# Performance work log

Measured on AMD Instinct MI355X. Metric: run time of the kernel, lower is better.

## Reference

```python
import jax, jax.numpy as jnp
import numpy as np

B, H, S, D = 8, 16, 1024, 64  # batch, heads, seq, projection_size = state_size // n_heads
SCALE = 1.0 / float(np.sqrt(D))


def setup_inputs() -> dict:
    key = jax.random.key(0)
    kq, kk, kv, kl = jax.random.split(key, 4)
    q = jax.random.normal(kq, (B, H, S, D), jnp.float32)
    k = jax.random.normal(kk, (B, H, S, D), jnp.float32)
    v = jax.random.normal(kv, (B, H, S, D), jnp.float32)
    # causal position mask: True = masked (filled with -inf), as in masked_fill
    position_mask = jnp.triu(jnp.ones((S, S), dtype=bool), k=1)
    # per-batch source lengths in [S//2, S]; mask positions >= length
    lengths = jax.random.randint(kl, (B,), S // 2, S + 1)
    src_length_mask = jnp.arange(S)[None, :] >= lengths[:, None]  # [B, S]
    return {"q": q, "k": k, "v": v,
            "position_mask": position_mask,
            "src_length_mask": src_length_mask}


def reference(q, q_unused=None, *, _=None, **__):
    raise RuntimeError  # placeholder (replaced below)


def reference(q, k, v, position_mask, src_length_mask):
    # scores = scale * Q K^T   (torch: bmm over [B*H, S, D]; here kept 4D, same math)
    logits = jnp.einsum('bhqd,bhkd->bhqk', q, k) * SCALE  # [B,H,Sq,Sk]
    neg_inf = jnp.array(-jnp.inf, dtype=logits.dtype)
    # apply_logit_masks: position mask broadcasts over [B,H],
    # src_length_mask viewed as [B,1,1,Sk]
    logits = jnp.where(position_mask[None, None, :, :], neg_inf, logits)
    logits = jnp.where(src_length_mask[:, None, None, :], neg_inf, logits)
    att = jax.nn.softmax(logits, axis=-1)
    # dropout is identity in eval mode; _attention_read: bmm(scores, v)
    out = jnp.einsum('bhqk,bhkd->bhqd', att, v)  # [B,H,Sq,D]
    return out
```

## Files before the change

kernel.cpp:

```cpp
#include <hip/hip_runtime.h>
#include <stdint.h>

#define B_ 8
#define H_ 16
#define S_ 1024
#define D_ 64
#define C1_ 0.18033688f
#define C2_ 23.08312065f
#define BHSD (B_ * H_ * S_ * D_)

typedef __attribute__((ext_vector_type(8))) short bf16x8;
typedef __attribute__((ext_vector_type(4))) float f32x4;
typedef __attribute__((ext_vector_type(4))) unsigned short us4;

__device__ __forceinline__ unsigned short f2bf(float f) {
  union { float f; uint32_t u; } v; v.f = f;
  return (unsigned short)((v.u + 0x7fffu + ((v.u >> 16) & 1u)) >> 16);
}
__device__ __forceinline__ uint32_t rne2(float a, float b) {
  union { float f; uint32_t u; } x, y; x.f = a; y.f = b;
  uint32_t ua = x.u + 0x7fffu + ((x.u >> 16) & 1u);
  uint32_t ub = y.u + 0x7fffu + ((y.u >> 16) & 1u);
  return (ua >> 16) | (ub & 0xFFFF0000u);
}
__device__ __forceinline__ uint32_t cvtpk(float lo, float hi) {
  uint32_t r;
  asm("v_cvt_pk_bf16_f32 %0, %1, %2" : "=v"(r) : "v"(lo), "v"(hi));
  return r;
}
__device__ __forceinline__ float fexp2(float x) {
#if __has_builtin(__builtin_amdgcn_exp2f)
  return __builtin_amdgcn_exp2f(x);
#else
  return exp2f(x);
#endif
}

__global__ __launch_bounds__(256) void prep_kv_kernel(
    const float* __restrict__ kg, const float* __restrict__ vg,
    unsigned short* __restrict__ kws, unsigned short* __restrict__ vtws) {
  __shared__ unsigned short t[64 * 68];
  const int tid = threadIdx.x;
  const int kt  = blockIdx.x & 15;
  const int bh  = blockIdx.x >> 4;
  const size_t off  = ((size_t)bh * S_ + kt * 64) * D_;
  const size_t tout = (size_t)(bh * 16 + kt) * 4096;
#pragma unroll
  for (int i = 0; i < 2; i++) {
    int c = tid + 256 * i;
    int nt = c >> 7, kc = (c >> 6) & 1, quad = (c >> 4) & 3, l16 = c & 15;
    int key = nt * 16 + l16, d0 = kc * 32 + quad * 8;
    const float4 a = *(const float4*)(kg + off + key * 64 + d0);
    const float4 b = *(const float4*)(kg + off + key * 64 + d0 + 4);
    uint4 o = make_uint4(rne2(a.x, a.y), rne2(a.z, a.w), rne2(b.x, b.y), rne2(b.z, b.w));
    *(uint4*)(kws + tout + (size_t)c * 8) = o;
  }
#pragma unroll
  for (int i = 0; i < 4; i++) {
    int c = tid + 256 * i;
    float4 val = *(const float4*)(vg + off + c * 4);
    int key = c >> 4, d0 = (c & 15) * 4;
    us4 o; o[0] = f2bf(val.x); o[1] = f2bf(val.y); o[2] = f2bf(val.z); o[3] = f2bf(val.w);
    *(us4*)(&t[key * 68 + d0]) = o;
  }
  __syncthreads();
#pragma unroll
  for (int i = 0; i < 2; i++) {
    int c = tid + 256 * i;
    int nt = c >> 7, kc = (c >> 6) & 1, quad = (c >> 4) & 3, l16 = c & 15;
    int d = nt * 16 + l16, kb2 = kc * 32 + quad * 4;
    bf16x8 o;
#pragma unroll
    for (int j = 0; j < 8; j++) {
      int key = kb2 + ((j >> 2) << 4) + (j & 3);
      o[j] = (short)t[key * 68 + d];
    }
    *(bf16x8*)(vtws + tout + (size_t)c * 8) = o;
  }
}

__global__ __launch_bounds__(256, 4) void attn_flash_kernel(
    const float* __restrict__ qg,
    const unsigned short* __restrict__ kws,
    const unsigned short* __restrict__ vtws,
    const void* __restrict__ posmask,
    const void* __restrict__ srcmask,
    float* __restrict__ outg)
{
  __shared__ unsigned short lds_k[2][4096];
  __shared__ unsigned short lds_v[2][4096];
  __shared__ int s_len;

  const int tid  = threadIdx.x;
  const int wave = tid >> 6;
  const int lane = tid & 63;
  const int quad = lane >> 4;
  const int l16  = lane & 15;

  const int p   = blockIdx.x;
  const int xcd = p & 7;
  const int si  = p >> 3;
  const int bh  = xcd * 16 + (si >> 3);
  const int tq  = (si + (si >> 5)) & 7;
  const int qb  = (tq & 1) ? (7 - (tq >> 1)) : (tq >> 1);
  const int b   = bh >> 4;

  const uint8_t* pmb = (const uint8_t*)posmask;
  const int mode = pmb[1] ? 0 : (pmb[2] ? 1 : (pmb[4] ? 2 : 3));

  if (tid == 0) s_len = S_;
  __syncthreads();
  {
    int lm = S_;
    for (int i = tid; i < S_; i += 256) {
      const int idx = b * S_ + i;
      bool masked;
      if (mode == 0)      masked = ((const uint8_t*) srcmask)[idx] != 0;
      else if (mode == 1) masked = ((const uint16_t*)srcmask)[idx] != 0;
      else                masked = ((const uint32_t*)srcmask)[idx] != 0;
      if (masked) lm = min(lm, i);
    }
    if (lm < S_) atomicMin(&s_len, lm);
  }
  __syncthreads();
  const int len = s_len;

  const unsigned short* kt0 = kws  + (size_t)bh * 16 * 4096;
  const unsigned short* vt0 = vtws + (size_t)bh * 16 * 4096;

  const int q0 = qb * 128;
  const int qw = q0 + wave * 32;

  bf16x8 qfrag[2][2];
#pragma unroll
  for (int g = 0; g < 2; g++)
#pragma unroll
    for (int kc = 0; kc < 2; kc++) {
      const float* qp = qg + ((size_t)bh * S_ + qw + g * 16 + l16) * D_ + kc * 32 + quad * 8;
      float4 a = *(const float4*)qp;
      float4 c = *(const float4*)(qp + 4);
      union { bf16x8 v; uint32_t u[4]; } u;
      u.u[0] = cvtpk(a.x, a.y); u.u[1] = cvtpk(a.z, a.w);
      u.u[2] = cvtpk(c.x, c.y); u.u[3] = cvtpk(c.z, c.w);
      qfrag[g][kc] = u.v;
    }

  f32x4 ofrag[2][4];
#pragma unroll
  for (int g = 0; g < 2; g++)
#pragma unroll
    for (int nt = 0; nt < 4; nt++) ofrag[g][nt] = (f32x4){0.f, 0.f, 0.f, 0.f};
  float l_i0 = 0.f, l_i1 = 0.f;

  const int kend  = min(q0 + 128, len);
  const int ntile = (kend + 63) >> 6;

  {
    *(bf16x8*)(&lds_k[0][tid * 8])         = *(const bf16x8*)(kt0 + (size_t)tid * 8);
    *(bf16x8*)(&lds_k[0][(tid + 256) * 8]) = *(const bf16x8*)(kt0 + (size_t)(tid + 256) * 8);
    *(bf16x8*)(&lds_v[0][tid * 8])         = *(const bf16x8*)(vt0 + (size_t)tid * 8);
    *(bf16x8*)(&lds_v[0][(tid + 256) * 8]) = *(const bf16x8*)(vt0 + (size_t)(tid + 256) * 8);
  }

  for (int kt = 0; kt < ntile; kt++) {
    const int k0  = kt * 64;
    const int buf = kt & 1;
    const bool more = (kt + 1 < ntile);

    __syncthreads();

    bf16x8 pk0, pk1, pv0, pv1;
    if (more) {
      const unsigned short* kp = kt0 + (size_t)(kt + 1) * 4096;
      const unsigned short* vp = vt0 + (size_t)(kt + 1) * 4096;
      pk0 = *(const bf16x8*)(kp + tid * 8);
      pk1 = *(const bf16x8*)(kp + (tid + 256) * 8);
      pv0 = *(const bf16x8*)(vp + tid * 8);
      pv1 = *(const bf16x8*)(vp + (tid + 256) * 8);
    }

    if (qw + 31 >= k0) {
      const int km0 = min(qw + l16, len - 1);
      const int km1 = min(qw + 16 + l16, len - 1);
      const bool need_mask = (k0 + 63 > qw) || (k0 + 64 > len);
      float rs0 = 0.f, rs1 = 0.f;
      union { bf16x8 v[2]; uint32_t u[8]; } pa0, pa1;
#pragma unroll
      for (int nt = 0; nt < 4; nt++) {
        f32x4 a0 = (f32x4){0.f, 0.f, 0.f, 0.f};
        f32x4 a1 = (f32x4){0.f, 0.f, 0.f, 0.f};
#pragma unroll
        for (int kc = 0; kc < 2; kc++) {
          bf16x8 kb = *(const bf16x8*)(&lds_k[buf][(((nt * 2 + kc) * 4 + quad) * 16 + l16) * 8]);
          a0 = __builtin_amdgcn_mfma_f32_16x16x32_bf16(kb, qfrag[0][kc], a0, 0, 0, 0);
          a1 = __builtin_amdgcn_mfma_f32_16x16x32_bf16(kb, qfrag[1][kc], a1, 0, 0, 0);
        }
        float e0[4], e1[4];
#pragma unroll
        for (int r = 0; r < 4; r++) {
          float x0 = fexp2(fmaf(a0[r], C1_, -C2_));
          float x1 = fexp2(fmaf(a1[r], C1_, -C2_));
          if (need_mask) {
            const int key = k0 + nt * 16 + quad * 4 + r;
            x0 = (key <= km0) ? x0 : 0.f;
            x1 = (key <= km1) ? x1 : 0.f;
          }
          e0[r] = x0; rs0 += x0;
          e1[r] = x1; rs1 += x1;
        }
        const int ui = (nt >> 1) * 4 + (nt & 1) * 2;
        pa0.u[ui]     = cvtpk(e0[0], e0[1]);
        pa0.u[ui + 1] = cvtpk(e0[2], e0[3]);
        pa1.u[ui]     = cvtpk(e1[0], e1[1]);
        pa1.u[ui + 1] = cvtpk(e1[2], e1[3]);
      }
      rs0 += __shfl_xor(rs0, 16); rs0 += __shfl_xor(rs0, 32); l_i0 += rs0;
      rs1 += __shfl_xor(rs1, 16); rs1 += __shfl_xor(rs1, 32); l_i1 += rs1;

#pragma unroll
      for (int nt = 0; nt < 4; nt++)
#pragma unroll
        for (int kc = 0; kc < 2; kc++) {
          bf16x8 vb = *(const bf16x8*)(&lds_v[buf][(((nt * 2 + kc) * 4 + quad) * 16 + l16) * 8]);
          ofrag[0][nt] = __builtin_amdgcn_mfma_f32_16x16x32_bf16(pa0.v[kc], vb, ofrag[0][nt], 0, 0, 0);
          ofrag[1][nt] = __builtin_amdgcn_mfma_f32_16x16x32_bf16(pa1.v[kc], vb, ofrag[1][nt], 0, 0, 0);
        }
    }

    if (more) {
      *(bf16x8*)(&lds_k[buf ^ 1][tid * 8])         = pk0;
      *(bf16x8*)(&lds_k[buf ^ 1][(tid + 256) * 8]) = pk1;
      *(bf16x8*)(&lds_v[buf ^ 1][tid * 8])         = pv0;
      *(bf16x8*)(&lds_v[buf ^ 1][(tid + 256) * 8]) = pv1;
    }
  }

#pragma unroll
  for (int g = 0; g < 2; g++)
#pragma unroll
    for (int r = 0; r < 4; r++) {
      float l = __shfl(g ? l_i1 : l_i0, quad * 4 + r);
      float inv = (l > 0.f) ? 1.0f / l : 0.f;
      const int qrow2 = qw + g * 16 + quad * 4 + r;
      float* orow = outg + ((size_t)bh * S_ + qrow2) * D_;
#pragma unroll
      for (int nt = 0; nt < 4; nt++)
        orow[nt * 16 + l16] = ofrag[g][nt][r] * inv;
    }
}

extern "C" void kernel_launch(void* const* d_in, const int* in_sizes, int n_in,
                              void* d_out, int out_size, void* d_ws, size_t ws_size,
                              hipStream_t stream) {
  const float* q = (const float*)d_in[0];
  const float* k = (const float*)d_in[1];
  const float* v = (const float*)d_in[2];
  const void* posmask = d_in[3];
  const void* srcmask = d_in[4];
  float* out = (float*)d_out;

  unsigned short* kws  = (unsigned short*)d_ws;
  unsigned short* vtws = kws + (size_t)BHSD;

  hipLaunchKernelGGL(prep_kv_kernel, dim3(B_ * H_ * 16), dim3(256), 0, stream, k, v, kws, vtws);
  hipLaunchKernelGGL(attn_flash_kernel, dim3(B_ * H_ * 8), dim3(256), 0, stream,
                     q, kws, vtws, posmask, srcmask, out);
}
```

Before: 172.3 us.

## Batch QK MFMAs, raise wave priority, split LDS stores, per-wave length reduction

The source-length scan now uses a per-wave loop with a shuffle-based min reduction, which removes the shared atomic and two block barriers. The QK^T MFMAs for all four key subtiles are issued back to back ahead of the exp/softmax step, and both MFMA phases are wrapped in s_setprio so MFMA-issuing waves get scheduling preference. The K prefetch store into the next LDS buffer moves between the QK and softmax phases so it can overlap other work. The cost is higher register pressure from holding eight accumulator vectors, and each wave now reads the whole mask row instead of a quarter of it.

```diff
diff --git a/kernel.cpp b/kernel.cpp
--- a/kernel.cpp
+++ b/kernel.cpp
@@ -89,7 +89,6 @@
 {
   __shared__ unsigned short lds_k[2][4096];
   __shared__ unsigned short lds_v[2][4096];
-  __shared__ int s_len;
 
   const int tid  = threadIdx.x;
   const int wave = tid >> 6;
@@ -108,22 +107,22 @@
   const uint8_t* pmb = (const uint8_t*)posmask;
   const int mode = pmb[1] ? 0 : (pmb[2] ? 1 : (pmb[4] ? 2 : 3));
 
-  if (tid == 0) s_len = S_;
-  __syncthreads();
-  {
-    int lm = S_;
-    for (int i = tid; i < S_; i += 256) {
-      const int idx = b * S_ + i;
-      bool masked;
-      if (mode == 0)      masked = ((const uint8_t*) srcmask)[idx] != 0;
-      else if (mode == 1) masked = ((const uint16_t*)srcmask)[idx] != 0;
-      else                masked = ((const uint32_t*)srcmask)[idx] != 0;
-      if (masked) lm = min(lm, i);
-    }
-    if (lm < S_) atomicMin(&s_len, lm);
-  }
-  __syncthreads();
-  const int len = s_len;
+  int lm = S_;
+  for (int i = lane; i < S_; i += 64) {
+    const int idx = b * S_ + i;
+    bool masked;
+    if (mode == 0)      masked = ((const uint8_t*) srcmask)[idx] != 0;
+    else if (mode == 1) masked = ((const uint16_t*)srcmask)[idx] != 0;
+    else                masked = ((const uint32_t*)srcmask)[idx] != 0;
+    if (masked) lm = min(lm, i);
+  }
+  lm = min(lm, __shfl_xor(lm, 1));
+  lm = min(lm, __shfl_xor(lm, 2));
+  lm = min(lm, __shfl_xor(lm, 4));
+  lm = min(lm, __shfl_xor(lm, 8));
+  lm = min(lm, __shfl_xor(lm, 16));
+  lm = min(lm, __shfl_xor(lm, 32));
+  const int len = lm;
 
   const unsigned short* kt0 = kws  + (size_t)bh * 16 * 4096;
   const unsigned short* vt0 = vtws + (size_t)bh * 16 * 4096;
@@ -179,7 +178,33 @@
       pv1 = *(const bf16x8*)(vp + (tid + 256) * 8);
     }
 
-    if (qw + 31 >= k0) {
+    const bool live = (qw + 31 >= k0);
+
+    f32x4 a0[4], a1[4];
+    if (live) {
+#pragma unroll
+      for (int nt = 0; nt < 4; nt++) {
+        a0[nt] = (f32x4){0.f, 0.f, 0.f, 0.f};
+        a1[nt] = (f32x4){0.f, 0.f, 0.f, 0.f};
+      }
+      __builtin_amdgcn_s_setprio(1);
+#pragma unroll
+      for (int kc = 0; kc < 2; kc++)
+#pragma unroll
+        for (int nt = 0; nt < 4; nt++) {
+          bf16x8 kb = *(const bf16x8*)(&lds_k[buf][(((nt * 2 + kc) * 4 + quad) * 16 + l16) * 8]);
+          a0[nt] = __builtin_amdgcn_mfma_f32_16x16x32_bf16(kb, qfrag[0][kc], a0[nt], 0, 0, 0);
+          a1[nt] = __builtin_amdgcn_mfma_f32_16x16x32_bf16(kb, qfrag[1][kc], a1[nt], 0, 0, 0);
+        }
+      __builtin_amdgcn_s_setprio(0);
+    }
+
+    if (more) {
+      *(bf16x8*)(&lds_k[buf ^ 1][tid * 8])         = pk0;
+      *(bf16x8*)(&lds_k[buf ^ 1][(tid + 256) * 8]) = pk1;
+    }
+
+    if (live) {
       const int km0 = min(qw + l16, len - 1);
       const int km1 = min(qw + 16 + l16, len - 1);
       const bool need_mask = (k0 + 63 > qw) || (k0 + 64 > len);
@@ -187,19 +212,11 @@
       union { bf16x8 v[2]; uint32_t u[8]; } pa0, pa1;
 #pragma unroll
       for (int nt = 0; nt < 4; nt++) {
-        f32x4 a0 = (f32x4){0.f, 0.f, 0.f, 0.f};
-        f32x4 a1 = (f32x4){0.f, 0.f, 0.f, 0.f};
-#pragma unroll
-        for (int kc = 0; kc < 2; kc++) {
-          bf16x8 kb = *(const bf16x8*)(&lds_k[buf][(((nt * 2 + kc) * 4 + quad) * 16 + l16) * 8]);
-          a0 = __builtin_amdgcn_mfma_f32_16x16x32_bf16(kb, qfrag[0][kc], a0, 0, 0, 0);
-          a1 = __builtin_amdgcn_mfma_f32_16x16x32_bf16(kb, qfrag[1][kc], a1, 0, 0, 0);
-        }
         float e0[4], e1[4];
 #pragma unroll
         for (int r = 0; r < 4; r++) {
-          float x0 = fexp2(fmaf(a0[r], C1_, -C2_));
-          float x1 = fexp2(fmaf(a1[r], C1_, -C2_));
+          float x0 = fexp2(fmaf(a0[nt][r], C1_, -C2_));
+          float x1 = fexp2(fmaf(a1[nt][r], C1_, -C2_));
           if (need_mask) {
             const int key = k0 + nt * 16 + quad * 4 + r;
             x0 = (key <= km0) ? x0 : 0.f;
@@ -217,19 +234,19 @@
       rs0 += __shfl_xor(rs0, 16); rs0 += __shfl_xor(rs0, 32); l_i0 += rs0;
       rs1 += __shfl_xor(rs1, 16); rs1 += __shfl_xor(rs1, 32); l_i1 += rs1;
 
-#pragma unroll
-      for (int nt = 0; nt < 4; nt++)
-#pragma unroll
-        for (int kc = 0; kc < 2; kc++) {
+      __builtin_amdgcn_s_setprio(1);
+#pragma unroll
+      for (int kc = 0; kc < 2; kc++)
+#pragma unroll
+        for (int nt = 0; nt < 4; nt++) {
           bf16x8 vb = *(const bf16x8*)(&lds_v[buf][(((nt * 2 + kc) * 4 + quad) * 16 + l16) * 8]);
           ofrag[0][nt] = __builtin_amdgcn_mfma_f32_16x16x32_bf16(pa0.v[kc], vb, ofrag[0][nt], 0, 0, 0);
           ofrag[1][nt] = __builtin_amdgcn_mfma_f32_16x16x32_bf16(pa1.v[kc], vb, ofrag[1][nt], 0, 0, 0);
         }
+      __builtin_amdgcn_s_setprio(0);
     }
 
     if (more) {
-      *(bf16x8*)(&lds_k[buf ^ 1][tid * 8])         = pk0;
-      *(bf16x8*)(&lds_k[buf ^ 1][(tid + 256) * 8]) = pk1;
       *(bf16x8*)(&lds_v[buf ^ 1][tid * 8])         = pv0;
       *(bf16x8*)(&lds_v[buf ^ 1][(tid + 256) * 8]) = pv1;
     }
```

After: 229.3 us. 33.1% more time.

## Split attention into single-wave blocks reading K/V directly from global memory

Applied to the files above, without the earlier changes.

Each 256-thread block that shared double-buffered K/V tiles in LDS becomes a one-wave block that handles 32 query rows and loads K/V fragments straight from global memory (L2/L1). This drops the LDS staging, the block barriers and the shared atomicMin length scan, which becomes a wave shuffle reduction. Each wave now stops at its own causal bound instead of the 128-row block bound, and the finer grid gives better load balance. The cost is that four waves no longer share each K/V tile, so global and cache traffic rise, and every wave rescans the source mask.

```diff
diff --git a/kernel.cpp b/kernel.cpp
--- a/kernel.cpp
+++ b/kernel.cpp
@@ -79,7 +79,7 @@
   }
 }
 
-__global__ __launch_bounds__(256, 4) void attn_flash_kernel(
+__global__ __launch_bounds__(64, 4) void attn_flash_kernel(
     const float* __restrict__ qg,
     const unsigned short* __restrict__ kws,
     const unsigned short* __restrict__ vtws,
@@ -87,49 +87,41 @@
     const void* __restrict__ srcmask,
     float* __restrict__ outg)
 {
-  __shared__ unsigned short lds_k[2][4096];
-  __shared__ unsigned short lds_v[2][4096];
-  __shared__ int s_len;
-
-  const int tid  = threadIdx.x;
-  const int wave = tid >> 6;
-  const int lane = tid & 63;
+  const int lane = threadIdx.x;
   const int quad = lane >> 4;
   const int l16  = lane & 15;
 
   const int p   = blockIdx.x;
   const int xcd = p & 7;
-  const int si  = p >> 3;
-  const int bh  = xcd * 16 + (si >> 3);
-  const int tq  = (si + (si >> 5)) & 7;
-  const int qb  = (tq & 1) ? (7 - (tq >> 1)) : (tq >> 1);
+  const int i   = p >> 3;
+  const int bh  = xcd * 16 + (i >> 5);
+  const int j   = i & 31;
+  const int ws  = (j & 1) ? (31 - (j >> 1)) : (j >> 1);
+  const int qw  = ws * 32;
   const int b   = bh >> 4;
 
   const uint8_t* pmb = (const uint8_t*)posmask;
   const int mode = pmb[1] ? 0 : (pmb[2] ? 1 : (pmb[4] ? 2 : 3));
 
-  if (tid == 0) s_len = S_;
-  __syncthreads();
-  {
-    int lm = S_;
-    for (int i = tid; i < S_; i += 256) {
-      const int idx = b * S_ + i;
-      bool masked;
-      if (mode == 0)      masked = ((const uint8_t*) srcmask)[idx] != 0;
-      else if (mode == 1) masked = ((const uint16_t*)srcmask)[idx] != 0;
-      else                masked = ((const uint32_t*)srcmask)[idx] != 0;
-      if (masked) lm = min(lm, i);
-    }
-    if (lm < S_) atomicMin(&s_len, lm);
-  }
-  __syncthreads();
-  const int len = s_len;
+  int lm = S_;
+  for (int ii = lane; ii < S_; ii += 64) {
+    const int idx = b * S_ + ii;
+    bool masked;
+    if (mode == 0)      masked = ((const uint8_t*) srcmask)[idx] != 0;
+    else if (mode == 1) masked = ((const uint16_t*)srcmask)[idx] != 0;
+    else                masked = ((const uint32_t*)srcmask)[idx] != 0;
+    if (masked) lm = min(lm, ii);
+  }
+  lm = min(lm, __shfl_xor(lm, 1));
+  lm = min(lm, __shfl_xor(lm, 2));
+  lm = min(lm, __shfl_xor(lm, 4));
+  lm = min(lm, __shfl_xor(lm, 8));
+  lm = min(lm, __shfl_xor(lm, 16));
+  lm = min(lm, __shfl_xor(lm, 32));
+  const int len = lm;
 
   const unsigned short* kt0 = kws  + (size_t)bh * 16 * 4096;
   const unsigned short* vt0 = vtws + (size_t)bh * 16 * 4096;
-
-  const int q0 = qb * 128;
-  const int qw = q0 + wave * 32;
 
   bf16x8 qfrag[2][2];
 #pragma unroll
@@ -152,54 +144,46 @@
     for (int nt = 0; nt < 4; nt++) ofrag[g][nt] = (f32x4){0.f, 0.f, 0.f, 0.f};
   float l_i0 = 0.f, l_i1 = 0.f;
 
-  const int kend  = min(q0 + 128, len);
+  const int km0 = min(qw + l16, len - 1);
+  const int km1 = min(qw + 16 + l16, len - 1);
+
+  const int kend  = min(qw + 32, len);
   const int ntile = (kend + 63) >> 6;
 
-  {
-    *(bf16x8*)(&lds_k[0][tid * 8])         = *(const bf16x8*)(kt0 + (size_t)tid * 8);
-    *(bf16x8*)(&lds_k[0][(tid + 256) * 8]) = *(const bf16x8*)(kt0 + (size_t)(tid + 256) * 8);
-    *(bf16x8*)(&lds_v[0][tid * 8])         = *(const bf16x8*)(vt0 + (size_t)tid * 8);
-    *(bf16x8*)(&lds_v[0][(tid + 256) * 8]) = *(const bf16x8*)(vt0 + (size_t)(tid + 256) * 8);
-  }
-
   for (int kt = 0; kt < ntile; kt++) {
-    const int k0  = kt * 64;
-    const int buf = kt & 1;
-    const bool more = (kt + 1 < ntile);
-
-    __syncthreads();
-
-    bf16x8 pk0, pk1, pv0, pv1;
-    if (more) {
-      const unsigned short* kp = kt0 + (size_t)(kt + 1) * 4096;
-      const unsigned short* vp = vt0 + (size_t)(kt + 1) * 4096;
-      pk0 = *(const bf16x8*)(kp + tid * 8);
-      pk1 = *(const bf16x8*)(kp + (tid + 256) * 8);
-      pv0 = *(const bf16x8*)(vp + tid * 8);
-      pv1 = *(const bf16x8*)(vp + (tid + 256) * 8);
-    }
-
-    if (qw + 31 >= k0) {
-      const int km0 = min(qw + l16, len - 1);
-      const int km1 = min(qw + 16 + l16, len - 1);
-      const bool need_mask = (k0 + 63 > qw) || (k0 + 64 > len);
-      float rs0 = 0.f, rs1 = 0.f;
-      union { bf16x8 v[2]; uint32_t u[8]; } pa0, pa1;
-#pragma unroll
-      for (int nt = 0; nt < 4; nt++) {
-        f32x4 a0 = (f32x4){0.f, 0.f, 0.f, 0.f};
-        f32x4 a1 = (f32x4){0.f, 0.f, 0.f, 0.f};
+    const int k0 = kt * 64;
+    const unsigned short* kp = kt0 + (size_t)kt * 4096;
+    const unsigned short* vp = vt0 + (size_t)kt * 4096;
+    const bool need_mask = (k0 + 63 > qw) || (k0 + 64 > len);
+
+    float rs0 = 0.f, rs1 = 0.f;
+    union { bf16x8 v[2]; uint32_t u[8]; } pa0, pa1;
+
+#pragma unroll
+    for (int h = 0; h < 2; h++) {
+      bf16x8 kb[4];
+#pragma unroll
+      for (int nt2 = 0; nt2 < 2; nt2++)
 #pragma unroll
         for (int kc = 0; kc < 2; kc++) {
-          bf16x8 kb = *(const bf16x8*)(&lds_k[buf][(((nt * 2 + kc) * 4 + quad) * 16 + l16) * 8]);
-          a0 = __builtin_amdgcn_mfma_f32_16x16x32_bf16(kb, qfrag[0][kc], a0, 0, 0, 0);
-          a1 = __builtin_amdgcn_mfma_f32_16x16x32_bf16(kb, qfrag[1][kc], a1, 0, 0, 0);
+          const int nt = h * 2 + nt2;
+          kb[nt2 * 2 + kc] =
+              *(const bf16x8*)(kp + (((nt * 2 + kc) * 4 + quad) * 16 + l16) * 8);
         }
+#pragma unroll
+      for (int nt2 = 0; nt2 < 2; nt2++) {
+        const int nt = h * 2 + nt2;
+        f32x4 A0 = (f32x4){0.f, 0.f, 0.f, 0.f};
+        f32x4 A1 = (f32x4){0.f, 0.f, 0.f, 0.f};
+        A0 = __builtin_amdgcn_mfma_f32_16x16x32_bf16(kb[nt2 * 2 + 0], qfrag[0][0], A0, 0, 0, 0);
+        A1 = __builtin_amdgcn_mfma_f32_16x16x32_bf16(kb[nt2 * 2 + 0], qfrag[1][0], A1, 0, 0, 0);
+        A0 = __builtin_amdgcn_mfma_f32_16x16x32_bf16(kb[nt2 * 2 + 1], qfrag[0][1], A0, 0, 0, 0);
+        A1 = __builtin_amdgcn_mfma_f32_16x16x32_bf16(kb[nt2 * 2 + 1], qfrag[1][1], A1, 0, 0, 0);
         float e0[4], e1[4];
 #pragma unroll
         for (int r = 0; r < 4; r++) {
-          float x0 = fexp2(fmaf(a0[r], C1_, -C2_));
-          float x1 = fexp2(fmaf(a1[r], C1_, -C2_));
+          float x0 = fexp2(fmaf(A0[r], C1_, -C2_));
+          float x1 = fexp2(fmaf(A1[r], C1_, -C2_));
           if (need_mask) {
             const int key = k0 + nt * 16 + quad * 4 + r;
             x0 = (key <= km0) ? x0 : 0.f;
@@ -214,24 +198,21 @@
         pa1.u[ui]     = cvtpk(e1[0], e1[1]);
         pa1.u[ui + 1] = cvtpk(e1[2], e1[3]);
       }
-      rs0 += __shfl_xor(rs0, 16); rs0 += __shfl_xor(rs0, 32); l_i0 += rs0;
-      rs1 += __shfl_xor(rs1, 16); rs1 += __shfl_xor(rs1, 32); l_i1 += rs1;
-
+    }
+    rs0 += __shfl_xor(rs0, 16); rs0 += __shfl_xor(rs0, 32); l_i0 += rs0;
+    rs1 += __shfl_xor(rs1, 16); rs1 += __shfl_xor(rs1, 32); l_i1 += rs1;
+
+#pragma unroll
+    for (int kc = 0; kc < 2; kc++) {
+      bf16x8 vb[4];
 #pragma unroll
       for (int nt = 0; nt < 4; nt++)
-#pragma unroll
-        for (int kc = 0; kc < 2; kc++) {
-          bf16x8 vb = *(const bf16x8*)(&lds_v[buf][(((nt * 2 + kc) * 4 + quad) * 16 + l16) * 8]);
-          ofrag[0][nt] = __builtin_amdgcn_mfma_f32_16x16x32_bf16(pa0.v[kc], vb, ofrag[0][nt], 0, 0, 0);
-          ofrag[1][nt] = __builtin_amdgcn_mfma_f32_16x16x32_bf16(pa1.v[kc], vb, ofrag[1][nt], 0, 0, 0);
-        }
-    }
-
-    if (more) {
-      *(bf16x8*)(&lds_k[buf ^ 1][tid * 8])         = pk0;
-      *(bf16x8*)(&lds_k[buf ^ 1][(tid + 256) * 8]) = pk1;
-      *(bf16x8*)(&lds_v[buf ^ 1][tid * 8])         = pv0;
-      *(bf16x8*)(&lds_v[buf ^ 1][(tid + 256) * 8]) = pv1;
+        vb[nt] = *(const bf16x8*)(vp + (((nt * 2 + kc) * 4 + quad) * 16 + l16) * 8);
+#pragma unroll
+      for (int nt = 0; nt < 4; nt++) {
+        ofrag[0][nt] = __builtin_amdgcn_mfma_f32_16x16x32_bf16(pa0.v[kc], vb[nt], ofrag[0][nt], 0, 0, 0);
+        ofrag[1][nt] = __builtin_amdgcn_mfma_f32_16x16x32_bf16(pa1.v[kc], vb[nt], ofrag[1][nt], 0, 0, 0);
+      }
     }
   }
 
@@ -263,6 +244,6 @@
   unsigned short* vtws = kws + (size_t)BHSD;
 
   hipLaunchKernelGGL(prep_kv_kernel, dim3(B_ * H_ * 16), dim3(256), 0, stream, k, v, kws, vtws);
-  hipLaunchKernelGGL(attn_flash_kernel, dim3(B_ * H_ * 8), dim3(256), 0, stream,
+  hipLaunchKernelGGL(attn_flash_kernel, dim3(B_ * H_ * 8 * 4), dim3(64), 0, stream,
                      q, kws, vtws, posmask, srcmask, out);
 }
```

Result: slower. 190.8 us (+10.8%).
